# Kernel optimization log

Hardware: AMD Instinct MI355X
Metric: run time of the kernel (lower is better)

The kernel has to match this reference:

```python
import jax, jax.numpy as jnp
import numpy as np

B = 128      # graphs
N = 32       # atoms per graph (fixed)
NODES = B * N
E = B * N * N  # fully-connected edges incl. self-loops
H = 256      # hidden_dim
TD = 128     # time_dim
TYPE = 100   # type_dim
NF = 10      # frac_emb_freq
EDGE_DIM = NF * 2 * 3 + 6  # 66
L = 4        # num_layers
EPS = 1e-5


def _edges():
    idx = jnp.arange(NODES).reshape(B, N)
    ei = jnp.broadcast_to(idx[:, :, None], (B, N, N)).reshape(-1)  # row (target)
    ej = jnp.broadcast_to(idx[:, None, :], (B, N, N)).reshape(-1)  # col (source)
    return ei, ej


def _layernorm(x, g, b):
    mu = jnp.mean(x, axis=-1, keepdims=True)
    var = jnp.mean((x - mu) ** 2, axis=-1, keepdims=True)
    return (x - mu) * jax.lax.rsqrt(var + EPS) * g + b


def setup_inputs() -> dict:
    key = jax.random.key(0)
    ks = jax.random.split(key, 32)
    p = lambda k, shp: (jax.random.normal(k, shp, dtype=jnp.float32) * 0.02)
    inp = {
        "t": jax.random.uniform(ks[0], (B,), dtype=jnp.float32),
        "atom_types": jax.random.normal(ks[1], (NODES, TYPE), dtype=jnp.float32),
        "frac_coords": jax.random.uniform(ks[2], (NODES, 3), dtype=jnp.float32),
        "l_polar": jax.random.normal(ks[3], (B, 6), dtype=jnp.float32),
        "node2graph": jnp.repeat(jnp.arange(B, dtype=jnp.int32), N),
        # type_smooth
        "Ws": p(ks[4], (TYPE, H)), "bs": jnp.zeros((H,), jnp.float32),
        # node_embedding
        "Wn": p(ks[5], (H + TD, H)), "bn": jnp.zeros((H,), jnp.float32),
        # per-layer params, stacked over L
        "ln_g": jnp.ones((L, H), jnp.float32), "ln_b": jnp.zeros((L, H), jnp.float32),
        "m1_W": p(ks[6], (L, 2 * H + EDGE_DIM, H)), "m1_b": jnp.zeros((L, H), jnp.float32),
        "m2_W": p(ks[7], (L, H, H)), "m2_b": jnp.zeros((L, H), jnp.float32),
        "a1_W": p(ks[8], (L, 2 * H, H)), "a1_b": jnp.zeros((L, H), jnp.float32),
        "a2_W": p(ks[9], (L, H, H)), "a2_b": jnp.zeros((L, H), jnp.float32),
        # final layer norm + readouts
        "fln_g": jnp.ones((H,), jnp.float32), "fln_b": jnp.zeros((H,), jnp.float32),
        "type_W": p(ks[10], (H, TYPE)), "type_b": jnp.zeros((TYPE,), jnp.float32),
        "polar_W": p(ks[11], (H, 6)),
        "frac_W": p(ks[12], (H, 3)),
    }
    return inp


def reference(t, atom_types, frac_coords, l_polar, node2graph,
              Ws, bs, Wn, bn, ln_g, ln_b, m1_W, m1_b, m2_W, m2_b,
              a1_W, a1_b, a2_W, a2_b, fln_g, fln_b, type_W, type_b,
              polar_W, frac_W):
    ei, ej = _edges()
    edge2graph = node2graph[ei]

    # ---- node features: type_smooth + sinusoidal time embedding ----
    half = TD // 2
    tfreq = jnp.exp(jnp.arange(half, dtype=jnp.float32) * (-np.log(10000.0) / (half - 1)))
    targ = t[:, None] * tfreq[None, :]                       # [B, half]
    time_emb = jnp.concatenate([jnp.sin(targ), jnp.cos(targ)], axis=-1)  # [B, TD]
    time_emb = jnp.repeat(time_emb, N, axis=0)               # [NODES, TD]
    type_emb = atom_types @ Ws + bs                           # [NODES, H]
    nf = jnp.concatenate([type_emb, time_emb], axis=-1) @ Wn + bn  # [NODES, H]

    # ---- edge features: sinusoidal frac-diff embedding + l_polar ----
    d = jnp.mod(frac_coords[ej] - frac_coords[ei], 1.0)       # [E, 3]
    ffreq = 2.0 * np.pi * jnp.arange(NF, dtype=jnp.float32)
    femb = (d[:, :, None] * ffreq[None, None, :]).reshape(E, NF * 3)
    femb = jnp.concatenate([jnp.sin(femb), jnp.cos(femb)], axis=-1)  # [E, 60]
    ef = jnp.concatenate([femb, l_polar[edge2graph]], axis=-1)       # [E, 66]

    # ---- GNN layers ----
    ones = jnp.ones((E,), jnp.float32)
    cnt = jax.ops.segment_sum(ones, ei, num_segments=NODES)          # [NODES]
    cnt = jnp.maximum(cnt, 1.0)[:, None]
    for i in range(L):
        h = _layernorm(nf, ln_g[i], ln_b[i])
        mij = jnp.concatenate([h[ei], h[ej], ef], axis=-1)           # [E, 2H+66]
        mij = jax.nn.silu(mij @ m1_W[i] + m1_b[i])
        mij = jax.nn.silu(mij @ m2_W[i] + m2_b[i])                   # [E, H]
        msg = jax.ops.segment_sum(mij, ei, num_segments=NODES) / cnt  # scatter-mean
        a = jnp.concatenate([nf, msg], axis=-1)
        a = jax.nn.silu(a @ a1_W[i] + a1_b[i])
        a = jax.nn.silu(a @ a2_W[i] + a2_b[i])
        nf = nf + a

    nf = _layernorm(nf, fln_g, fln_b)
    gsum = jax.ops.segment_sum(nf, node2graph, num_segments=B)
    gcnt = jnp.maximum(jax.ops.segment_sum(jnp.ones((NODES,), jnp.float32), node2graph, num_segments=B), 1.0)
    graph_features = gsum / gcnt[:, None]

    type_pred = nf @ type_W + type_b
    l_polar_pred = graph_features @ polar_W
    frac_coords_pred = nf @ frac_W
    return type_pred, l_polar_pred, frac_coords_pred
```

## Files before the change

### kernel.cpp

```cpp
#include <hip/hip_runtime.h>
#include <hip/hip_bf16.h>

typedef __attribute__((ext_vector_type(8))) short short8;
typedef __attribute__((ext_vector_type(4))) short short4v;
typedef __attribute__((ext_vector_type(4))) float float4v;
typedef __bf16 bf16x8 __attribute__((ext_vector_type(8)));

#define MFMA16(A,B,C) __builtin_amdgcn_mfma_f32_16x16x32_bf16( \
    __builtin_bit_cast(bf16x8,(A)), __builtin_bit_cast(bf16x8,(B)), (C), 0, 0, 0)

static __device__ __forceinline__ float bf2f(unsigned short b){
  unsigned u = ((unsigned)b) << 16; float f; __builtin_memcpy(&f,&u,sizeof(f)); return f;
}
static __device__ __forceinline__ unsigned short f2bf(float f){
  __bf16 h = (__bf16)f;
  return __builtin_bit_cast(unsigned short, h);
}
static __device__ __forceinline__ float siluf(float x){
  return x * __builtin_amdgcn_rcpf(1.0f + __expf(-x));
}
static __device__ __forceinline__ float ldf(const float* p, size_t i){ return p[i]; }
static __device__ __forceinline__ float ldf(const unsigned short* p, size_t i){ return bf2f(p[i]); }

__global__ __launch_bounds__(256) void k_gemm(
    const unsigned short* __restrict__ A, int lda,
    const unsigned short* __restrict__ Bp, int KT, int NT,
    const float* __restrict__ bias,
    float* __restrict__ outF, int ldoF,
    unsigned short* __restrict__ outH, int ldoH,
    const float* __restrict__ res,
    int Nc, int flags)
{
  const int w = threadIdx.x >> 6, lane = threadIdx.x & 63;
  const int l15 = lane & 15, q = lane >> 4;
  const int rowL = blockIdx.x * 64 + w * 16;
  const int colB = blockIdx.y * 64;
  const short8* pa = (const short8*)(A + (size_t)(rowL + l15) * lda);
  const short8* pb = (const short8*)Bp;
  float4v acc[4] = {};
  int ntc[4];
  #pragma unroll
  for (int i = 0; i < 4; ++i){ int t = (colB >> 4) + i; ntc[i] = t < NT ? t : NT - 1; }
  for (int kt = 0; kt < KT; ++kt){
    short8 a = pa[kt * 4 + q];
    #pragma unroll
    for (int i = 0; i < 4; ++i){
      short8 b = pb[(size_t)(kt * NT + ntc[i]) * 64 + lane];
      acc[i] = MFMA16(a, b, acc[i]);
    }
  }
  const bool doB = flags & 2, doS = flags & 1, doR = flags & 4;
  #pragma unroll
  for (int i = 0; i < 4; ++i){
    int c = colB + i * 16 + l15;
    if (c >= Nc) continue;
    float bv = doB ? bias[c] : 0.0f;
    #pragma unroll
    for (int r = 0; r < 4; ++r){
      int row = rowL + q * 4 + r;
      float v = acc[i][r] + bv;
      if (doS) v = siluf(v);
      if (doR) v += res[(size_t)row * ldoF + c];
      if (outF) outF[(size_t)row * ldoF + c] = v;
      if (outH) outH[(size_t)row * ldoH + c] = f2bf(v);
    }
  }
}

template<typename T>
static __device__ __forceinline__ void pack_tile(
    const T* W, int ldw, int Krows, int Ncols,
    unsigned short* dst, int NTtot, int ntoff, int kt, int nt,
    const float* addrow)
{
  int lane = threadIdx.x;
  int l15 = lane & 15, q = lane >> 4;
  int col = nt * 16 + l15;
  int kr0 = kt * 32 + q * 8;
  short8 v;
  #pragma unroll
  for (int j = 0; j < 8; ++j){
    int r = kr0 + j;
    float x = 0.0f;
    if (r < Krows && col < Ncols){
      x = ldf(W, (size_t)r * ldw + col);
      if (addrow) x += addrow[(r >> 5) * 256 + col];
    }
    v[j] = (short)f2bf(x);
  }
  ((short8*)dst)[(size_t)(kt * NTtot + ntoff + nt) * 64 + lane] = v;
}

__global__ void k_packW(
    const float* Ws, const float* Wn,
    const float* typeW, const float* polarW, const float* fracW,
    const float* m1W, const float* m2W, const float* a1W, const float* a2W,
    unsigned short* Wsp, unsigned short* Wnp, unsigned short* typep,
    unsigned short* polarp, unsigned short* fracp,
    unsigned short* W12p, unsigned short* W1botp, unsigned short* W2Tp,
    unsigned short* a1p, unsigned short* a2p)
{
  int b = blockIdx.x;
  if (b < 64)      { pack_tile(Ws,    256, 100, 256, Wsp,   16, 0, b >> 4, b & 15, nullptr); return; }
  if (b < 256){ int s = b - 64;  pack_tile(Wn,    256, 384, 256, Wnp,   12 == 12 ? 16 : 16, 0, s >> 4, s & 15, nullptr); return; }
  if (b < 312){ int s = b - 256; pack_tile(typeW, 100, 256, 100, typep,  7, 0, s / 7,  s % 7,  nullptr); return; }
  if (b < 320){ int s = b - 312; pack_tile(polarW,  6, 256,   6, polarp, 1, 0, s, 0, nullptr); return; }
  if (b < 328){ int s = b - 320; pack_tile(fracW,   3, 256,   3, fracp,  1, 0, s, 0, nullptr); return; }
  int s2 = b - 328;
  int l = s2 / 800, bb = s2 % 800;
  const float* m1Wl = m1W + (size_t)l * 578 * 256;
  const float* m2Wl = m2W + (size_t)l * 65536;
  const float* a1Wl = a1W + (size_t)l * 131072;
  const float* a2Wl = a2W + (size_t)l * 65536;
  unsigned short* W12pl   = W12p   + (size_t)l * 131072;
  unsigned short* W1botpl = W1botp + (size_t)l * 16384;
  unsigned short* W2Tpl   = W2Tp   + (size_t)l * 65536;
  unsigned short* a1pl    = a1p    + (size_t)l * 131072;
  unsigned short* a2pl    = a2p    + (size_t)l * 65536;
  if (bb < 128)       pack_tile(m1Wl,           256, 256, 256, W12pl,  32,  0, bb >> 4, bb & 15, nullptr);
  else if (bb < 256){ int s = bb - 128; pack_tile(m1Wl + 256*256, 256, 256, 256, W12pl,  32, 16, s >> 4, s & 15, nullptr); }
  else if (bb < 288){ int s = bb - 256; pack_tile(m1Wl + 512*256, 256,  64, 256, W1botpl,16,  0, s >> 4, s & 15, nullptr); }
  else if (bb < 416){ int s = bb - 288; pack_tile(m2Wl,           256, 256, 256, W2Tpl,  16,  0, s >> 4, s & 15, nullptr); }
  else if (bb < 672){ int s = bb - 416; pack_tile(a1Wl,           256, 512, 256, a1pl,   16,  0, s >> 4, s & 15, nullptr); }
  else              { int s = bb - 672; pack_tile(a2Wl,           256, 256, 256, a2pl,   16,  0, s >> 4, s & 15, nullptr); }
}

__global__ void k_prep2(const float* at, const float* t, const float* fc,
                        const float* lpol, const float* m1W, const float* m1b,
                        unsigned short* atp, unsigned short* cat1,
                        unsigned short* femb, float* lpw)
{
  int b = blockIdx.x;
  if (b < 2048){
    int id = b * 256 + threadIdx.x;
    int r = id >> 7, c = id & 127;
    atp[id] = (c < 100) ? f2bf(at[r * 100 + c]) : (unsigned short)0;
  } else if (b < 2176){
    int g = b - 2048, i = threadIdx.x;
    if (i < 128){
      float tg = t[g];
      int f = i & 63;
      float fr = __expf((-9.210340371976184f / 63.0f) * (float)f);
      float arg = tg * fr;
      float v = (i < 64) ? __sinf(arg) : __cosf(arg);
      unsigned short hv = f2bf(v);
      for (int n = 0; n < 32; ++n)
        cat1[(size_t)(g * 32 + n) * 384 + 256 + i] = hv;
    }
  } else if (b < 2688){
    int e = (b - 2176) * 256 + threadIdx.x;
    int g = e >> 10, i = (e >> 5) & 31, j = e & 31;
    int nt = g * 32 + i, ns = g * 32 + j;
    unsigned short o[64];
    #pragma unroll
    for (int k = 0; k < 3; ++k){
      float d = fc[ns * 3 + k] - fc[nt * 3 + k];
      d -= floorf(d);
      #pragma unroll
      for (int f = 0; f < 10; ++f){
        float ang = d * (6.283185307179586f * (float)f);
        o[k * 10 + f]      = f2bf(__sinf(ang));
        o[30 + k * 10 + f] = f2bf(__cosf(ang));
      }
    }
    #pragma unroll
    for (int z = 60; z < 64; ++z) o[z] = 0;
    short8* dst = (short8*)(femb + (size_t)e * 64);
    #pragma unroll
    for (int v = 0; v < 8; ++v){
      short8 s;
      #pragma unroll
      for (int j2 = 0; j2 < 8; ++j2) s[j2] = (short)o[v * 8 + j2];
      dst[v] = s;
    }
  } else {
    int s = b - 2688;
    int l = s >> 7, g = s & 127, c = threadIdx.x;
    const float* W = m1W + (size_t)l * 578 * 256;
    float acc = m1b[l * 256 + c];
    #pragma unroll
    for (int k = 0; k < 6; ++k)
      acc += lpol[g * 6 + k] * W[(572 + k) * 256 + c];
    lpw[((size_t)l * 128 + g) * 256 + c] = acc;
  }
}

#define HLD 264

__global__ __launch_bounds__(256) void k_lnP(
    const float* __restrict__ nf, const float* __restrict__ g_,
    const float* __restrict__ b_,
    const unsigned short* __restrict__ W12p, const float* __restrict__ lpwl,
    unsigned short* __restrict__ P1Tp, unsigned short* __restrict__ P2Tp)
{
  __shared__ unsigned short hld[32 * HLD];
  __shared__ unsigned short PT[256 * 40];
  const int w = threadIdx.x >> 6, lane = threadIdx.x & 63;
  const int l15 = lane & 15, q = lane >> 4;
  const int g = blockIdx.x >> 1, halfT = blockIdx.x & 1;
  #pragma unroll
  for (int rr = 0; rr < 8; ++rr){
    int row = w * 8 + rr;
    float4v x = *(const float4v*)(nf + ((size_t)(g*32+row))*256 + lane*4);
    float s = x[0]+x[1]+x[2]+x[3];
    #pragma unroll
    for (int m=1;m<64;m<<=1) s += __shfl_xor(s,m,64);
    float mu = s * (1.f/256.f);
    float d0=x[0]-mu,d1=x[1]-mu,d2=x[2]-mu,d3=x[3]-mu;
    float vs=d0*d0+d1*d1+d2*d2+d3*d3;
    #pragma unroll
    for (int m=1;m<64;m<<=1) vs += __shfl_xor(vs,m,64);
    float rs = rsqrtf(vs*(1.f/256.f)+1e-5f);
    float4v gg = *(const float4v*)(g_ + lane*4);
    float4v bb = *(const float4v*)(b_ + lane*4);
    short4v o;
    o[0]=(short)f2bf(d0*rs*gg[0]+bb[0]);
    o[1]=(short)f2bf(d1*rs*gg[1]+bb[1]);
    o[2]=(short)f2bf(d2*rs*gg[2]+bb[2]);
    o[3]=(short)f2bf(d3*rs*gg[3]+bb[3]);
    *(short4v*)(&hld[row*HLD + lane*4]) = o;
  }
  __syncthreads();
  float4v acc[2][4] = {};
  const short8* pb = (const short8*)W12p;
  for (int kt = 0; kt < 8; ++kt){
    short8 a0 = *(const short8*)(&hld[(size_t)l15*HLD + kt*32 + q*8]);
    short8 a1 = *(const short8*)(&hld[(size_t)(16+l15)*HLD + kt*32 + q*8]);
    #pragma unroll
    for (int i = 0; i < 4; ++i){
      short8 bfr = pb[(size_t)(kt*32 + halfT*16 + w*4 + i)*64 + lane];
      acc[0][i] = MFMA16(a0, bfr, acc[0][i]);
      acc[1][i] = MFMA16(a1, bfr, acc[1][i]);
    }
  }
  #pragma unroll
  for (int i = 0; i < 4; ++i){
    int Tl = w*4 + i;
    float lv = (halfT == 0) ? lpwl[g*256 + Tl*16 + l15] : 0.0f;
    #pragma unroll
    for (int mt = 0; mt < 2; ++mt){
      short4v o;
      #pragma unroll
      for (int r = 0; r < 4; ++r) o[r] = (short)f2bf(acc[mt][i][r] + lv);
      *(short4v*)(&PT[(size_t)(Tl*16 + l15)*40 + mt*16 + q*4]) = o;
    }
  }
  __syncthreads();
  unsigned short* dstbase = halfT ? P2Tp : P1Tp;
  #pragma unroll
  for (int s = 0; s < 4; ++s){
    int Tl = w + s*4;
    short8 v = *(const short8*)(&PT[(size_t)(Tl*16 + l15)*40 + q*8]);
    *(short8*)(dstbase + ((size_t)(g*16 + Tl)*64 + lane)*8) = v;
  }
}

__global__ __launch_bounds__(256) void k_a12(
    const unsigned short* __restrict__ cat2,
    const unsigned short* __restrict__ a1pl, const float* __restrict__ a1bl,
    const unsigned short* __restrict__ a2pl, const float* __restrict__ a2bl,
    float* __restrict__ nf, unsigned short* __restrict__ cat2w)
{
  __shared__ unsigned short t1[16 * HLD];
  const int w = threadIdx.x >> 6, lane = threadIdx.x & 63;
  const int l15 = lane & 15, q = lane >> 4;
  const int r0 = blockIdx.x * 16;
  const short8* pb1 = (const short8*)a1pl;
  const short8* pb2 = (const short8*)a2pl;
  float4v acc[4] = {};
  for (int kt = 0; kt < 16; ++kt){
    short8 a0 = *(const short8*)(cat2 + (size_t)(r0 + l15)*512 + kt*32 + q*8);
    #pragma unroll
    for (int i = 0; i < 4; ++i){
      short8 bfr = pb1[(size_t)(kt*16 + w*4 + i)*64 + lane];
      acc[i] = MFMA16(a0, bfr, acc[i]);
    }
  }
  #pragma unroll
  for (int i = 0; i < 4; ++i){
    int c = (w*4+i)*16 + l15;
    float bv = a1bl[c];
    #pragma unroll
    for (int r = 0; r < 4; ++r)
      t1[(size_t)(q*4 + r)*HLD + c] = f2bf(siluf(acc[i][r] + bv));
  }
  __syncthreads();
  float4v c2[4] = {};
  for (int kt = 0; kt < 8; ++kt){
    short8 a0 = *(const short8*)(&t1[(size_t)l15*HLD + kt*32 + q*8]);
    #pragma unroll
    for (int i = 0; i < 4; ++i){
      short8 bfr = pb2[(size_t)(kt*16 + w*4 + i)*64 + lane];
      c2[i] = MFMA16(a0, bfr, c2[i]);
    }
  }
  #pragma unroll
  for (int i = 0; i < 4; ++i){
    int c = (w*4+i)*16 + l15;
    float bv = a2bl[c];
    #pragma unroll
    for (int r = 0; r < 4; ++r){
      int row = r0 + q*4 + r;
      float v = nf[(size_t)row*256 + c] + siluf(c2[i][r] + bv);
      nf[(size_t)row*256 + c] = v;
      cat2w[(size_t)row*512 + c] = f2bf(v);
    }
  }
}

__global__ __launch_bounds__(256) void k_lnF(
    const float* __restrict__ nf, const float* __restrict__ g_,
    const float* __restrict__ b_,
    unsigned short* __restrict__ h, unsigned short* __restrict__ gf)
{
  __shared__ unsigned short hld[32 * HLD];
  const int w = threadIdx.x >> 6, lane = threadIdx.x & 63;
  const int g = blockIdx.x;
  #pragma unroll
  for (int rr = 0; rr < 8; ++rr){
    int row = w * 8 + rr;
    float4v x = *(const float4v*)(nf + ((size_t)(g*32+row))*256 + lane*4);
    float s = x[0]+x[1]+x[2]+x[3];
    #pragma unroll
    for (int m=1;m<64;m<<=1) s += __shfl_xor(s,m,64);
    float mu = s * (1.f/256.f);
    float d0=x[0]-mu,d1=x[1]-mu,d2=x[2]-mu,d3=x[3]-mu;
    float vs=d0*d0+d1*d1+d2*d2+d3*d3;
    #pragma unroll
    for (int m=1;m<64;m<<=1) vs += __shfl_xor(vs,m,64);
    float rs = rsqrtf(vs*(1.f/256.f)+1e-5f);
    float4v gg = *(const float4v*)(g_ + lane*4);
    float4v bb = *(const float4v*)(b_ + lane*4);
    short4v o;
    o[0]=(short)f2bf(d0*rs*gg[0]+bb[0]);
    o[1]=(short)f2bf(d1*rs*gg[1]+bb[1]);
    o[2]=(short)f2bf(d2*rs*gg[2]+bb[2]);
    o[3]=(short)f2bf(d3*rs*gg[3]+bb[3]);
    *(short4v*)(&hld[row*HLD + lane*4]) = o;
    *(short4v*)(h + ((size_t)(g*32+row))*256 + lane*4) = o;
  }
  __syncthreads();
  int c = threadIdx.x;
  float s = 0.0f;
  #pragma unroll
  for (int n = 0; n < 32; ++n) s += bf2f(hld[n*HLD + c]);
  gf[g*256 + c] = f2bf(s * (1.0f/32.0f));
}

#define EST 268
__global__ __launch_bounds__(256, 4) void k_edge(
    const unsigned short* __restrict__ femb,
    const unsigned short* __restrict__ W1botp,
    const unsigned short* __restrict__ P1Tp,
    const unsigned short* __restrict__ P2Tp,
    const unsigned short* __restrict__ W2Tp,
    const float* __restrict__ b2,
    unsigned short* __restrict__ cat2)
{
  __shared__ unsigned short M1[64 * EST];
  const int w = threadIdx.x >> 6, lane = threadIdx.x & 63;
  const int l15 = lane & 15, q = lane >> 4;
  const int b = blockIdx.x, g = b >> 4;
  const int n0 = (b & 15) * 2;
  const int cb = w * 64;
  const short8* fb8  = (const short8*)femb;
  const short8* w1b8 = (const short8*)W1botp;
  const short8* p1t8 = (const short8*)P1Tp;
  const short8* p2t8 = (const short8*)P2Tp;
  const short8* w2t8 = (const short8*)W2Tp;

  short8 ohj[2], ohn[2];
  #pragma unroll
  for (int p = 0; p < 2; ++p){
    int tj = p * 16 + l15;
    int tn = n0 + p;
    #pragma unroll
    for (int j = 0; j < 8; ++j){
      ohj[p][j] = (short)((q * 8 + j) == tj ? 0x3F80 : 0);
      ohn[p][j] = (short)((q * 8 + j) == tn ? 0x3F80 : 0);
    }
  }

  float4v acc[4][4] = {};
  #pragma unroll
  for (int ks = 0; ks < 4; ++ks){
    short8 a[4];
    #pragma unroll
    for (int ct = 0; ct < 4; ++ct){
      int nt = w * 4 + ct;
      if (ks < 2)       a[ct] = w1b8[(size_t)(ks * 16 + nt) * 64 + lane];
      else if (ks == 2) a[ct] = p2t8[(size_t)(g * 16 + nt) * 64 + lane];
      else              a[ct] = p1t8[(size_t)(g * 16 + nt) * 64 + lane];
    }
    #pragma unroll
    for (int et = 0; et < 4; ++et){
      short8 bf;
      if (ks < 2){
        int edge = b * 64 + et * 16 + l15;
        bf = fb8[(size_t)edge * 8 + ks * 4 + q];
      } else if (ks == 2) bf = ohj[et & 1];
      else                bf = ohn[et >> 1];
      #pragma unroll
      for (int ct = 0; ct < 4; ++ct)
        acc[ct][et] = MFMA16(a[ct], bf, acc[ct][et]);
    }
  }
  #pragma unroll
  for (int ct = 0; ct < 4; ++ct)
    #pragma unroll
    for (int et = 0; et < 4; ++et){
      short4v sv;
      #pragma unroll
      for (int r = 0; r < 4; ++r) sv[r] = (short)f2bf(siluf(acc[ct][et][r]));
      *(short4v*)(&M1[(size_t)(et * 16 + l15) * EST + cb + ct * 16 + q * 4]) = sv;
    }
  __syncthreads();
  float4v c2[4][4] = {};
  for (int kt = 0; kt < 8; ++kt){
    short8 a[4];
    #pragma unroll
    for (int ct = 0; ct < 4; ++ct)
      a[ct] = w2t8[(size_t)(kt * 16 + w * 4 + ct) * 64 + lane];
    #pragma unroll
    for (int et = 0; et < 4; ++et){
      short8 m = *(const short8*)(&M1[(size_t)(et * 16 + l15) * EST + kt * 32 + q * 8]);
      #pragma unroll
      for (int ct = 0; ct < 4; ++ct)
        c2[ct][et] = MFMA16(m, a[ct], c2[ct][et]);
    }
  }
  #pragma unroll
  for (int ct = 0; ct < 4; ++ct){
    float bv = b2[cb + ct * 16 + l15];
    #pragma unroll
    for (int nn = 0; nn < 2; ++nn){
      float s = siluf(c2[ct][2*nn  ][0] + bv) + siluf(c2[ct][2*nn  ][1] + bv)
              + siluf(c2[ct][2*nn  ][2] + bv) + siluf(c2[ct][2*nn  ][3] + bv)
              + siluf(c2[ct][2*nn+1][0] + bv) + siluf(c2[ct][2*nn+1][1] + bv)
              + siluf(c2[ct][2*nn+1][2] + bv) + siluf(c2[ct][2*nn+1][3] + bv);
      s += __shfl_xor(s, 16, 64);
      s += __shfl_xor(s, 32, 64);
      if (q == 0)
        cat2[(size_t)(b*2 + nn) * 512 + 256 + cb + ct * 16 + l15] =
            f2bf(s * (1.0f / 32.0f));
    }
  }
}

extern "C" void kernel_launch(void* const* d_in, const int* in_sizes, int n_in,
                              void* d_out, int out_size, void* d_ws, size_t ws_size,
                              hipStream_t stream)
{
  const float* t      = (const float*)d_in[0];
  const float* at     = (const float*)d_in[1];
  const float* fc     = (const float*)d_in[2];
  const float* lpol   = (const float*)d_in[3];
  const float* Ws     = (const float*)d_in[5];
  const float* bs     = (const float*)d_in[6];
  const float* Wn     = (const float*)d_in[7];
  const float* bn     = (const float*)d_in[8];
  const float* ln_g   = (const float*)d_in[9];
  const float* ln_b   = (const float*)d_in[10];
  const float* m1W    = (const float*)d_in[11];
  const float* m1b    = (const float*)d_in[12];
  const float* m2W    = (const float*)d_in[13];
  const float* m2b    = (const float*)d_in[14];
  const float* a1W    = (const float*)d_in[15];
  const float* a1b    = (const float*)d_in[16];
  const float* a2W    = (const float*)d_in[17];
  const float* a2b    = (const float*)d_in[18];
  const float* flng   = (const float*)d_in[19];
  const float* flnb   = (const float*)d_in[20];
  const float* typeW  = (const float*)d_in[21];
  const float* typeb  = (const float*)d_in[22];
  const float* polarW = (const float*)d_in[23];
  const float* fracW  = (const float*)d_in[24];
  float* out = (float*)d_out;

  char* ws = (char*)d_ws;
  size_t off = 0;
  auto alloc = [&](size_t bytes) -> char* {
    char* p = ws + off; off += (bytes + 255) & ~(size_t)255; return p;
  };
  float*          nf    = (float*)         alloc((size_t)4096*256*4);
  unsigned short* cat2  = (unsigned short*)alloc((size_t)4096*512*2);
  unsigned short* h     = (unsigned short*)alloc((size_t)4096*256*2);
  unsigned short* cat1  = (unsigned short*)alloc((size_t)4096*384*2);
  unsigned short* atp   = (unsigned short*)alloc((size_t)4096*128*2);
  unsigned short* femb  = (unsigned short*)alloc((size_t)131072*64*2);
  float*          lpw   = (float*)         alloc((size_t)4*128*256*4);
  unsigned short* P1Tp  = (unsigned short*)alloc((size_t)128*16*64*8*2);
  unsigned short* P2Tp  = (unsigned short*)alloc((size_t)128*16*64*8*2);
  unsigned short* gf    = (unsigned short*)alloc((size_t)128*256*2);
  unsigned short* Wsp   = (unsigned short*)alloc((size_t)4*16*1024);
  unsigned short* Wnp   = (unsigned short*)alloc((size_t)12*16*1024);
  unsigned short* typep = (unsigned short*)alloc((size_t)8*7*1024);
  unsigned short* polarp= (unsigned short*)alloc((size_t)8*1*1024);
  unsigned short* fracp = (unsigned short*)alloc((size_t)8*1*1024);
  unsigned short* W12p  = (unsigned short*)alloc((size_t)4*131072*2);
  unsigned short* W1botp= (unsigned short*)alloc((size_t)4*16384*2);
  unsigned short* W2Tp  = (unsigned short*)alloc((size_t)4*65536*2);
  unsigned short* a1p   = (unsigned short*)alloc((size_t)4*131072*2);
  unsigned short* a2p   = (unsigned short*)alloc((size_t)4*65536*2);

  k_packW<<<dim3(3528), dim3(64), 0, stream>>>(Ws, Wn, typeW, polarW, fracW,
      m1W, m2W, a1W, a2W,
      Wsp, Wnp, typep, polarp, fracp, W12p, W1botp, W2Tp, a1p, a2p);
  k_prep2<<<dim3(3200), dim3(256), 0, stream>>>(at, t, fc, lpol, m1W, m1b,
                                                atp, cat1, femb, lpw);
  k_gemm<<<dim3(64,4), dim3(256), 0, stream>>>(atp, 128, Wsp, 4, 16, bs,
      (float*)nullptr, 0, cat1, 384, (const float*)nullptr, 256, 2);
  k_gemm<<<dim3(64,4), dim3(256), 0, stream>>>(cat1, 384, Wnp, 12, 16, bn,
      nf, 256, cat2, 512, (const float*)nullptr, 256, 2);

  for (int l = 0; l < 4; ++l){
    k_lnP<<<dim3(256), dim3(256), 0, stream>>>(nf, ln_g + l*256, ln_b + l*256,
        W12p + (size_t)l*131072, lpw + (size_t)l*32768, P1Tp, P2Tp);
    k_edge<<<dim3(2048), dim3(256), 0, stream>>>(femb, W1botp + (size_t)l*16384,
        P1Tp, P2Tp, W2Tp + (size_t)l*65536, m2b + l*256, cat2);
    k_a12<<<dim3(256), dim3(256), 0, stream>>>(cat2, a1p + (size_t)l*131072,
        a1b + l*256, a2p + (size_t)l*65536, a2b + l*256, nf, cat2);
  }

  k_lnF<<<dim3(128), dim3(256), 0, stream>>>(nf, flng, flnb, h, gf);
  k_gemm<<<dim3(64,2), dim3(256), 0, stream>>>(h, 256, typep, 8, 7, typeb,
      out, 100, (unsigned short*)nullptr, 0, (const float*)nullptr, 100, 2);
  k_gemm<<<dim3(2,1), dim3(256), 0, stream>>>(gf, 256, polarp, 8, 1,
      (const float*)nullptr, out + 409600, 6, (unsigned short*)nullptr, 0,
      (const float*)nullptr, 6, 0);
  k_gemm<<<dim3(64,1), dim3(256), 0, stream>>>(h, 256, fracp, 8, 1,
      (const float*)nullptr, out + 410368, 3, (unsigned short*)nullptr, 0,
      (const float*)nullptr, 3, 0);
}
```

Measured before the change: 370.4 us.

## Add per-node projections in edge epilogue instead of one-hot MFMA; use 8 waves

The edge kernel stops folding the per-node projections P1/P2 into the first GEMM through one-hot MFMA K-steps, cutting that GEMM from four K-steps to two. It instead loads P1/P2 rows directly and adds them in the SiLU epilogue. P1/P2 change from a packed transposed tile layout to a plain row-major node-by-channel layout, written with scalar stores from k_lnP, so the LDS transpose and one barrier there are dropped. k_edge also moves to 512 threads (8 waves, 32 channels each), halving per-wave accumulators to raise occupancy, at the cost of scattered 2-byte stores in k_lnP and more redundant weight loads per block.

```diff
diff --git a/kernel.cpp b/kernel.cpp
--- a/kernel.cpp
+++ b/kernel.cpp
@@ -102,7 +102,7 @@
 {
   int b = blockIdx.x;
   if (b < 64)      { pack_tile(Ws,    256, 100, 256, Wsp,   16, 0, b >> 4, b & 15, nullptr); return; }
-  if (b < 256){ int s = b - 64;  pack_tile(Wn,    256, 384, 256, Wnp,   12 == 12 ? 16 : 16, 0, s >> 4, s & 15, nullptr); return; }
+  if (b < 256){ int s = b - 64;  pack_tile(Wn,    256, 384, 256, Wnp,   16, 0, s >> 4, s & 15, nullptr); return; }
   if (b < 312){ int s = b - 256; pack_tile(typeW, 100, 256, 100, typep,  7, 0, s / 7,  s % 7,  nullptr); return; }
   if (b < 320){ int s = b - 312; pack_tile(polarW,  6, 256,   6, polarp, 1, 0, s, 0, nullptr); return; }
   if (b < 328){ int s = b - 320; pack_tile(fracW,   3, 256,   3, fracp,  1, 0, s, 0, nullptr); return; }
@@ -191,10 +191,9 @@
     const float* __restrict__ nf, const float* __restrict__ g_,
     const float* __restrict__ b_,
     const unsigned short* __restrict__ W12p, const float* __restrict__ lpwl,
-    unsigned short* __restrict__ P1Tp, unsigned short* __restrict__ P2Tp)
+    unsigned short* __restrict__ P1, unsigned short* __restrict__ P2)
 {
   __shared__ unsigned short hld[32 * HLD];
-  __shared__ unsigned short PT[256 * 40];
   const int w = threadIdx.x >> 6, lane = threadIdx.x & 63;
   const int l15 = lane & 15, q = lane >> 4;
   const int g = blockIdx.x >> 1, halfT = blockIdx.x & 1;
@@ -233,25 +232,19 @@
       acc[1][i] = MFMA16(a1, bfr, acc[1][i]);
     }
   }
+  unsigned short* dst = halfT ? P2 : P1;
   #pragma unroll
   for (int i = 0; i < 4; ++i){
-    int Tl = w*4 + i;
-    float lv = (halfT == 0) ? lpwl[g*256 + Tl*16 + l15] : 0.0f;
+    int ch = (w*4 + i)*16 + l15;
+    float lv = (halfT == 0) ? lpwl[g*256 + ch] : 0.0f;
     #pragma unroll
     for (int mt = 0; mt < 2; ++mt){
-      short4v o;
       #pragma unroll
-      for (int r = 0; r < 4; ++r) o[r] = (short)f2bf(acc[mt][i][r] + lv);
-      *(short4v*)(&PT[(size_t)(Tl*16 + l15)*40 + mt*16 + q*4]) = o;
-    }
-  }
-  __syncthreads();
-  unsigned short* dstbase = halfT ? P2Tp : P1Tp;
-  #pragma unroll
-  for (int s = 0; s < 4; ++s){
-    int Tl = w + s*4;
-    short8 v = *(const short8*)(&PT[(size_t)(Tl*16 + l15)*40 + q*8]);
-    *(short8*)(dstbase + ((size_t)(g*16 + Tl)*64 + lane)*8) = v;
+      for (int r = 0; r < 4; ++r){
+        int node = g*32 + mt*16 + q*4 + r;
+        dst[(size_t)node*256 + ch] = f2bf(acc[mt][i][r] + lv);
+      }
+    }
   }
 }
 
@@ -348,11 +341,11 @@
 }
 
 #define EST 268
-__global__ __launch_bounds__(256, 4) void k_edge(
+__global__ __launch_bounds__(512, 8) void k_edge(
     const unsigned short* __restrict__ femb,
     const unsigned short* __restrict__ W1botp,
-    const unsigned short* __restrict__ P1Tp,
-    const unsigned short* __restrict__ P2Tp,
+    const unsigned short* __restrict__ P1,
+    const unsigned short* __restrict__ P2,
     const unsigned short* __restrict__ W2Tp,
     const float* __restrict__ b2,
     unsigned short* __restrict__ cat2)
@@ -362,75 +355,66 @@
   const int l15 = lane & 15, q = lane >> 4;
   const int b = blockIdx.x, g = b >> 4;
   const int n0 = (b & 15) * 2;
-  const int cb = w * 64;
+  const int cb = w * 32;
   const short8* fb8  = (const short8*)femb;
   const short8* w1b8 = (const short8*)W1botp;
-  const short8* p1t8 = (const short8*)P1Tp;
-  const short8* p2t8 = (const short8*)P2Tp;
   const short8* w2t8 = (const short8*)W2Tp;
 
-  short8 ohj[2], ohn[2];
-  #pragma unroll
-  for (int p = 0; p < 2; ++p){
-    int tj = p * 16 + l15;
-    int tn = n0 + p;
-    #pragma unroll
-    for (int j = 0; j < 8; ++j){
-      ohj[p][j] = (short)((q * 8 + j) == tj ? 0x3F80 : 0);
-      ohn[p][j] = (short)((q * 8 + j) == tn ? 0x3F80 : 0);
-    }
-  }
-
-  float4v acc[4][4] = {};
-  #pragma unroll
-  for (int ks = 0; ks < 4; ++ks){
-    short8 a[4];
-    #pragma unroll
-    for (int ct = 0; ct < 4; ++ct){
-      int nt = w * 4 + ct;
-      if (ks < 2)       a[ct] = w1b8[(size_t)(ks * 16 + nt) * 64 + lane];
-      else if (ks == 2) a[ct] = p2t8[(size_t)(g * 16 + nt) * 64 + lane];
-      else              a[ct] = p1t8[(size_t)(g * 16 + nt) * 64 + lane];
-    }
+  short4v p1v[2][2], p2v[2][2];
+  #pragma unroll
+  for (int ct = 0; ct < 2; ++ct){
+    int co = cb + ct*16 + q*4;
+    p1v[0][ct] = *(const short4v*)(P1 + (size_t)(g*32 + n0    )*256 + co);
+    p1v[1][ct] = *(const short4v*)(P1 + (size_t)(g*32 + n0 + 1)*256 + co);
+    p2v[0][ct] = *(const short4v*)(P2 + (size_t)(g*32 +      l15)*256 + co);
+    p2v[1][ct] = *(const short4v*)(P2 + (size_t)(g*32 + 16 + l15)*256 + co);
+  }
+
+  float4v acc[2][4] = {};
+  #pragma unroll
+  for (int ks = 0; ks < 2; ++ks){
+    short8 a[2];
+    #pragma unroll
+    for (int ct = 0; ct < 2; ++ct)
+      a[ct] = w1b8[(size_t)(ks * 16 + w * 2 + ct) * 64 + lane];
     #pragma unroll
     for (int et = 0; et < 4; ++et){
-      short8 bf;
-      if (ks < 2){
-        int edge = b * 64 + et * 16 + l15;
-        bf = fb8[(size_t)edge * 8 + ks * 4 + q];
-      } else if (ks == 2) bf = ohj[et & 1];
-      else                bf = ohn[et >> 1];
+      int edge = b * 64 + et * 16 + l15;
+      short8 bf = fb8[(size_t)edge * 8 + ks * 4 + q];
       #pragma unroll
-      for (int ct = 0; ct < 4; ++ct)
+      for (int ct = 0; ct < 2; ++ct)
         acc[ct][et] = MFMA16(a[ct], bf, acc[ct][et]);
     }
   }
   #pragma unroll
-  for (int ct = 0; ct < 4; ++ct)
+  for (int ct = 0; ct < 2; ++ct)
     #pragma unroll
     for (int et = 0; et < 4; ++et){
       short4v sv;
       #pragma unroll
-      for (int r = 0; r < 4; ++r) sv[r] = (short)f2bf(siluf(acc[ct][et][r]));
+      for (int r = 0; r < 4; ++r){
+        float v = acc[ct][et][r] + bf2f(p1v[et>>1][ct][r]) + bf2f(p2v[et&1][ct][r]);
+        sv[r] = (short)f2bf(siluf(v));
+      }
       *(short4v*)(&M1[(size_t)(et * 16 + l15) * EST + cb + ct * 16 + q * 4]) = sv;
     }
   __syncthreads();
-  float4v c2[4][4] = {};
+  float4v c2[2][4] = {};
   for (int kt = 0; kt < 8; ++kt){
-    short8 a[4];
-    #pragma unroll
-    for (int ct = 0; ct < 4; ++ct)
-      a[ct] = w2t8[(size_t)(kt * 16 + w * 4 + ct) * 64 + lane];
+    short8 a[2];
+    #pragma unroll
+    for (int ct = 0; ct < 2; ++ct)
+      a[ct] = w2t8[(size_t)(kt * 16 + w * 2 + ct) * 64 + lane];
     #pragma unroll
     for (int et = 0; et < 4; ++et){
       short8 m = *(const short8*)(&M1[(size_t)(et * 16 + l15) * EST + kt * 32 + q * 8]);
       #pragma unroll
-      for (int ct = 0; ct < 4; ++ct)
+      for (int ct = 0; ct < 2; ++ct)
         c2[ct][et] = MFMA16(m, a[ct], c2[ct][et]);
     }
   }
   #pragma unroll
-  for (int ct = 0; ct < 4; ++ct){
+  for (int ct = 0; ct < 2; ++ct){
     float bv = b2[cb + ct * 16 + l15];
     #pragma unroll
     for (int nn = 0; nn < 2; ++nn){
@@ -489,8 +473,8 @@
   unsigned short* atp   = (unsigned short*)alloc((size_t)4096*128*2);
   unsigned short* femb  = (unsigned short*)alloc((size_t)131072*64*2);
   float*          lpw   = (float*)         alloc((size_t)4*128*256*4);
-  unsigned short* P1Tp  = (unsigned short*)alloc((size_t)128*16*64*8*2);
-  unsigned short* P2Tp  = (unsigned short*)alloc((size_t)128*16*64*8*2);
+  unsigned short* P1    = (unsigned short*)alloc((size_t)4096*256*2);
+  unsigned short* P2    = (unsigned short*)alloc((size_t)4096*256*2);
   unsigned short* gf    = (unsigned short*)alloc((size_t)128*256*2);
   unsigned short* Wsp   = (unsigned short*)alloc((size_t)4*16*1024);
   unsigned short* Wnp   = (unsigned short*)alloc((size_t)12*16*1024);
@@ -515,9 +499,9 @@
 
   for (int l = 0; l < 4; ++l){
     k_lnP<<<dim3(256), dim3(256), 0, stream>>>(nf, ln_g + l*256, ln_b + l*256,
-        W12p + (size_t)l*131072, lpw + (size_t)l*32768, P1Tp, P2Tp);
-    k_edge<<<dim3(2048), dim3(256), 0, stream>>>(femb, W1botp + (size_t)l*16384,
-        P1Tp, P2Tp, W2Tp + (size_t)l*65536, m2b + l*256, cat2);
+        W12p + (size_t)l*131072, lpw + (size_t)l*32768, P1, P2);
+    k_edge<<<dim3(2048), dim3(512), 0, stream>>>(femb, W1botp + (size_t)l*16384,
+        P1, P2, W2Tp + (size_t)l*65536, m2b + l*256, cat2);
     k_a12<<<dim3(256), dim3(256), 0, stream>>>(cat2, a1p + (size_t)l*131072,
         a1b + l*256, a2p + (size_t)l*65536, a2b + l*256, nf, cat2);
   }
```

Result: slower. 407.1 us (+9.9%).
